# Kernel tuning notes

Hardware: AMD Instinct MI355X
Metric: run time of the kernel (lower is better)

The kernel has to match this reference:

```python
import jax, jax.numpy as jnp
import numpy as np

N, CIN, COUT, H, W = 32, 256, 256, 56, 56

def setup_inputs() -> dict:
    key = jax.random.key(0)
    k1, k2, k3 = jax.random.split(key, 3)
    x = jax.random.normal(k1, (N, CIN, H, W), dtype=jnp.float32)
    weight = jax.random.normal(k2, (COUT, CIN, 3, 3), dtype=jnp.float32) * 0.05
    bias = jax.random.normal(k3, (COUT,), dtype=jnp.float32)
    return {"x": x, "weight": weight, "bias": bias}

def reference(x, weight, bias):
    # 3x3 conv, stride=1, padding=1 (SAME), fused bias + ReLU.
    # Winograd F(2x2,3x3) is mathematically identical to direct conv.
    y = jax.lax.conv_general_dilated(
        x, weight,
        window_strides=(1, 1),
        padding=((1, 1), (1, 1)),
        dimension_numbers=("NCHW", "OIHW", "NCHW"),
    )
    return jax.nn.relu(y + bias[None, :, None, None])
```

## Files before the change

### kernel.cpp

```cpp
#include <hip/hip_runtime.h>


#define GLOBAL_AS __attribute__((address_space(1)))
#define LDS_AS __attribute__((address_space(3)))

typedef __attribute__((ext_vector_type(8))) short short8;
typedef __attribute__((ext_vector_type(4))) float f32x4;
typedef __attribute__((ext_vector_type(4))) unsigned int u32x4;

#define CIN   256
#define HWS   3136
#define PTOT  100352
#define KTOT  2304
#define WROWB 4608
#define ZPOFF 1179648
#define XTOFF 1310720
#define WSNEED (XTOFF + (size_t)PTOT * 512)

__device__ __forceinline__ unsigned short f2bf(float f) {
  unsigned u = __builtin_bit_cast(unsigned, f);
  return (unsigned short)((u + 0x7fffu + ((u >> 16) & 1u)) >> 16);
}

__global__ void wcvt_kernel(const float* __restrict__ w, unsigned char* __restrict__ ws) {
  if (blockIdx.x == 0 && threadIdx.x < 128)
    ((unsigned*)(ws + ZPOFF))[threadIdx.x] = 0u;
  int o = blockIdx.x * 256 + threadIdx.x;
  int co = o / KTOT;
  int rr = o - co * KTOT;
  int tap = rr >> 8;
  int ci = rr & 255;
  ((unsigned short*)ws)[o] = f2bf(w[co * KTOT + ci * 9 + tap]);
}

__global__ __launch_bounds__(256) void xcvt_kernel(const float* __restrict__ x,
                                                   unsigned char* __restrict__ ws) {
  __shared__ float lt[64 * 257];
  const int pg0 = blockIdx.x * 64;
  const int n   = pg0 / HWS;
  const int pi0 = pg0 - n * HWS;
  const int t   = threadIdx.x;
  {
    const int px = t & 63;
    const int cg = t >> 6;
    const float* xb = x + ((size_t)n * 256) * HWS + pi0 + px;
#pragma unroll 8
    for (int i = 0; i < 64; ++i) {
      const int c = i * 4 + cg;
      lt[px * 257 + c] = xb[(size_t)c * HWS];
    }
  }
  __syncthreads();
  {
    const int slot = t & 31;
    const int pxw  = t >> 5;
    unsigned char* xt = ws + XTOFF;
#pragma unroll
    for (int i = 0; i < 8; ++i) {
      const int p = i * 8 + pxw;
      const float* r = &lt[p * 257 + slot * 8];
      u32x4 v;
#pragma unroll
      for (int j = 0; j < 4; ++j)
        v[j] = (unsigned)f2bf(r[2 * j]) | ((unsigned)f2bf(r[2 * j + 1]) << 16);
      *(u32x4*)(xt + (size_t)(pg0 + p) * 512 + slot * 16) = v;
    }
  }
}

__global__ __launch_bounds__(256, 2) void conv_kernel(
    const unsigned char* __restrict__ ws, const float* __restrict__ bias,
    float* __restrict__ out) {
  __shared__ __align__(16) unsigned char smem[65536];

  const unsigned char* wb = ws;
  const unsigned char* xt = ws + XTOFF;
  const unsigned char* zp = ws + ZPOFF;

  const int bid = blockIdx.x;
  const int sw  = (bid & 7) * 196 + (bid >> 3);
  const int co0 = (sw & 1) * 128;
  const int p0  = (sw >> 1) * 128;

  const int t    = threadIdx.x;
  const int lane = t & 63;
  const int wave = t >> 6;
  const int wm   = wave & 1;
  const int wn   = wave >> 1;
  const int rl   = lane & 15;
  const int kq   = lane >> 4;
  const int l7   = lane & 7;
  const int l8   = lane >> 3;

  const unsigned chanoff = (unsigned)((l7 * 16) ^ ((l8 & 7) << 4));

  const unsigned char* aG[4];
  long long bG[4];
  int hB[4], wB[4];
#pragma unroll
  for (int i = 0; i < 4; ++i) {
    const int row = wave * 32 + i * 8 + l8;
    aG[i] = wb + (size_t)(co0 + row) * WROWB + chanoff;
    const int pg = p0 + row;
    const int n  = pg / HWS;
    const int pi = pg - n * HWS;
    hB[i] = pi / 56;
    wB[i] = pi - hB[i] * 56;
    bG[i] = (long long)pg * 512 + (long long)chanoff;
  }

  f32x4 acc[4][4];
  const f32x4 zero4 = {0.f, 0.f, 0.f, 0.f};
#pragma unroll
  for (int mi = 0; mi < 4; ++mi)
#pragma unroll
    for (int ni = 0; ni < 4; ++ni) acc[mi][ni] = zero4;

  auto stage = [&](int s, int buf) {
    const int cq  = s / 9;
    const int tap = s - cq * 9;
    const int kh  = tap / 3;
    const int dh  = kh - 1;
    const int dw  = (tap - kh * 3) - 1;
    const int koffA = tap * 512 + cq * 128;
    unsigned char* lb = smem + buf * 32768;
#pragma unroll
    for (int i = 0; i < 4; ++i) {
      __builtin_amdgcn_global_load_lds(
          (const GLOBAL_AS unsigned int*)(aG[i] + koffA),
          (LDS_AS unsigned int*)(lb + (wave * 4 + i) * 1024), 16, 0, 0);
    }
    const long long doff = (long long)(dh * 56 + dw) * 512 + cq * 128;
#pragma unroll
    for (int i = 0; i < 4; ++i) {
      const int hh = hB[i] + dh;
      const int wwi = wB[i] + dw;
      const bool ok = ((unsigned)hh < 56u) && ((unsigned)wwi < 56u);
      const unsigned char* g = ok ? (xt + bG[i] + doff) : zp;
      __builtin_amdgcn_global_load_lds(
          (const GLOBAL_AS unsigned int*)g,
          (LDS_AS unsigned int*)(lb + 16384 + (wave * 4 + i) * 1024), 16, 0, 0);
    }
  };

  unsigned offA[2], offB[2];
#pragma unroll
  for (int ks = 0; ks < 2; ++ks) {
    const unsigned koff = (unsigned)((kq * 16 + ks * 64) ^ (l7 << 4));
    offA[ks] = (unsigned)((wm * 64 + rl) * 128) + koff;
    offB[ks] = (unsigned)((wn * 64 + rl) * 128) + koff;
  }

  auto compute = [&](int buf) {
    const unsigned char* bA = smem + buf * 32768;
    const unsigned char* bB = bA + 16384;
#pragma unroll
    for (int ks = 0; ks < 2; ++ks) {
      short8 a[4], b[4];
#pragma unroll
      for (int mi = 0; mi < 4; ++mi)
        a[mi] = *(const short8*)(bA + offA[ks] + mi * 2048);
#pragma unroll
      for (int ni = 0; ni < 4; ++ni)
        b[ni] = *(const short8*)(bB + offB[ks] + ni * 2048);
#pragma unroll
      for (int mi = 0; mi < 4; ++mi)
#pragma unroll
        for (int ni = 0; ni < 4; ++ni)
          acc[mi][ni] = __builtin_amdgcn_mfma_f32_16x16x32_bf16(
              a[mi], b[ni], acc[mi][ni], 0, 0, 0);
    }
  };

  stage(0, 0);
  __syncthreads();
  int buf = 0;
  for (int s = 0; s < 36; ++s) {
    if (s < 35) stage(s + 1, buf ^ 1);
    compute(buf);
    __syncthreads();
    buf ^= 1;
  }

#pragma unroll
  for (int mi = 0; mi < 4; ++mi) {
    const int row = co0 + wm * 64 + mi * 16 + kq * 4;
    float br[4];
#pragma unroll
    for (int j = 0; j < 4; ++j) br[j] = bias[row + j];
#pragma unroll
    for (int ni = 0; ni < 4; ++ni) {
      const int pgb = p0 + wn * 64 + ni * 16;
      const int n   = pgb / HWS;
      const int pib = pgb - n * HWS;
#pragma unroll
      for (int j = 0; j < 4; ++j) {
        float v = acc[mi][ni][j] + br[j];
        out[(size_t)(n * 256 + row + j) * HWS + pib + rl] = fmaxf(v, 0.f);
      }
    }
  }
}

__global__ void naive_kernel(const float* __restrict__ x, const float* __restrict__ w,
                             const float* __restrict__ bias, float* __restrict__ out) {
  int idx = blockIdx.x * 256 + threadIdx.x;
  if (idx >= 32 * 256 * HWS) return;
  int n  = idx / (256 * HWS);
  int r  = idx - n * 256 * HWS;
  int co = r / HWS;
  int p  = r - co * HWS;
  int h = p / 56, ww = p - h * 56;
  float s = bias[co];
  const float* xb = x + (size_t)n * 256 * HWS;
  const float* wbp = w + (size_t)co * KTOT;
  for (int ci = 0; ci < 256; ++ci) {
    const float* xc = xb + (size_t)ci * HWS;
    const float* wc = wbp + ci * 9;
    for (int kh = 0; kh < 3; ++kh) {
      int hh = h + kh - 1;
      if ((unsigned)hh >= 56u) continue;
      for (int kw = 0; kw < 3; ++kw) {
        int w2 = ww + kw - 1;
        if ((unsigned)w2 >= 56u) continue;
        s += xc[hh * 56 + w2] * wc[kh * 3 + kw];
      }
    }
  }
  out[idx] = fmaxf(s, 0.f);
}

extern "C" void kernel_launch(void* const* d_in, const int* in_sizes, int n_in,
                              void* d_out, int out_size, void* d_ws, size_t ws_size,
                              hipStream_t stream) {
  const float* x    = (const float*)d_in[0];
  const float* w    = (const float*)d_in[1];
  const float* bias = (const float*)d_in[2];
  float* out        = (float*)d_out;

  if (ws_size < WSNEED) {
    hipLaunchKernelGGL(naive_kernel, dim3((32 * 256 * HWS + 255) / 256), dim3(256),
                       0, stream, x, w, bias, out);
    return;
  }
  unsigned char* ws = (unsigned char*)d_ws;
  hipLaunchKernelGGL(wcvt_kernel, dim3(2304), dim3(256), 0, stream, w, ws);
  hipLaunchKernelGGL(xcvt_kernel, dim3(PTOT / 64), dim3(256), 0, stream, x, ws);
  hipLaunchKernelGGL(conv_kernel, dim3(1568), dim3(256), 0, stream, ws, bias, out);
}
```

Baseline: 169.0 us.

## Deepen conv pipeline to 4 stages with half-size K chunks and setprio

Splits each K stage from 128 to 64 bytes per row (72 stages instead of 36) and replaces the double-buffered loop with a 4-buffer ring that prefetches three stages ahead. Each step uses explicit vmcnt waits plus s_barrier in place of __syncthreads, and wraps the MFMA block in s_setprio. The LDS swizzle and load mapping are rewritten for the 64-byte rows. The aim is to hide global-to-LDS latency more deeply and cut barrier stalls, at the cost of twice as many barriers and smaller MFMA bursts per sync.

```diff
diff --git a/kernel.cpp b/kernel.cpp
--- a/kernel.cpp
+++ b/kernel.cpp
@@ -89,24 +89,23 @@
   const int wn   = wave >> 1;
   const int rl   = lane & 15;
   const int kq   = lane >> 4;
-  const int l7   = lane & 7;
-  const int l8   = lane >> 3;
-
-  const unsigned chanoff = (unsigned)((l7 * 16) ^ ((l8 & 7) << 4));
-
-  const unsigned char* aG[4];
-  long long bG[4];
-  int hB[4], wB[4];
-#pragma unroll
-  for (int i = 0; i < 4; ++i) {
-    const int row = wave * 32 + i * 8 + l8;
-    aG[i] = wb + (size_t)(co0 + row) * WROWB + chanoff;
+  const int q2   = lane >> 2;
+
+  const unsigned jb = (unsigned)(((lane & 3) ^ ((lane >> 3) & 3)) * 16);
+
+  const unsigned char* aG[2];
+  long long bG[2];
+  int hB[2], wB[2];
+#pragma unroll
+  for (int i = 0; i < 2; ++i) {
+    const int row = i * 64 + wave * 16 + q2;
+    aG[i] = wb + (size_t)(co0 + row) * WROWB + jb;
     const int pg = p0 + row;
     const int n  = pg / HWS;
     const int pi = pg - n * HWS;
     hB[i] = pi / 56;
     wB[i] = pi - hB[i] * 56;
-    bG[i] = (long long)pg * 512 + (long long)chanoff;
+    bG[i] = (long long)pg * 512 + (long long)jb;
   }
 
   f32x4 acc[4][4];
@@ -122,65 +121,67 @@
     const int kh  = tap / 3;
     const int dh  = kh - 1;
     const int dw  = (tap - kh * 3) - 1;
-    const int koffA = tap * 512 + cq * 128;
-    unsigned char* lb = smem + buf * 32768;
-#pragma unroll
-    for (int i = 0; i < 4; ++i) {
+    const unsigned koffA = (unsigned)(tap * 512 + cq * 64);
+    unsigned char* lbA = smem + buf * 8192 + wave * 1024;
+    unsigned char* lbB = smem + 32768 + buf * 8192 + wave * 1024;
+#pragma unroll
+    for (int i = 0; i < 2; ++i)
       __builtin_amdgcn_global_load_lds(
           (const GLOBAL_AS unsigned int*)(aG[i] + koffA),
-          (LDS_AS unsigned int*)(lb + (wave * 4 + i) * 1024), 16, 0, 0);
-    }
-    const long long doff = (long long)(dh * 56 + dw) * 512 + cq * 128;
-#pragma unroll
-    for (int i = 0; i < 4; ++i) {
-      const int hh = hB[i] + dh;
+          (LDS_AS unsigned int*)(lbA + i * 4096), 16, 0, 0);
+    const long long doff = (long long)(dh * 56 + dw) * 512 + cq * 64;
+#pragma unroll
+    for (int i = 0; i < 2; ++i) {
+      const int hh  = hB[i] + dh;
       const int wwi = wB[i] + dw;
       const bool ok = ((unsigned)hh < 56u) && ((unsigned)wwi < 56u);
       const unsigned char* g = ok ? (xt + bG[i] + doff) : zp;
       __builtin_amdgcn_global_load_lds(
           (const GLOBAL_AS unsigned int*)g,
-          (LDS_AS unsigned int*)(lb + 16384 + (wave * 4 + i) * 1024), 16, 0, 0);
+          (LDS_AS unsigned int*)(lbB + i * 4096), 16, 0, 0);
     }
   };
 
-  unsigned offA[2], offB[2];
-#pragma unroll
-  for (int ks = 0; ks < 2; ++ks) {
-    const unsigned koff = (unsigned)((kq * 16 + ks * 64) ^ (l7 << 4));
-    offA[ks] = (unsigned)((wm * 64 + rl) * 128) + koff;
-    offB[ks] = (unsigned)((wn * 64 + rl) * 128) + koff;
-  }
-
-  auto compute = [&](int buf) {
-    const unsigned char* bA = smem + buf * 32768;
-    const unsigned char* bB = bA + 16384;
-#pragma unroll
-    for (int ks = 0; ks < 2; ++ks) {
-      short8 a[4], b[4];
-#pragma unroll
-      for (int mi = 0; mi < 4; ++mi)
-        a[mi] = *(const short8*)(bA + offA[ks] + mi * 2048);
-#pragma unroll
-      for (int ni = 0; ni < 4; ++ni)
-        b[ni] = *(const short8*)(bB + offB[ks] + ni * 2048);
-#pragma unroll
-      for (int mi = 0; mi < 4; ++mi)
-#pragma unroll
-        for (int ni = 0; ni < 4; ++ni)
-          acc[mi][ni] = __builtin_amdgcn_mfma_f32_16x16x32_bf16(
-              a[mi], b[ni], acc[mi][ni], 0, 0, 0);
-    }
-  };
+  const unsigned srd  = (unsigned)((kq ^ ((rl >> 1) & 3)) * 16);
+  const unsigned offA = (unsigned)((wm * 64 + rl) * 64) + srd;
+  const unsigned offB = (unsigned)((wn * 64 + rl) * 64) + srd;
+
+#define STEP(S, BUF, VM, DO_STAGE)                                           \
+  {                                                                          \
+    asm volatile("s_waitcnt vmcnt(" VM ")\n\ts_barrier" ::: "memory");       \
+    const unsigned char* bA = smem + (BUF) * 8192;                           \
+    const unsigned char* bB = smem + 32768 + (BUF) * 8192;                   \
+    short8 av[4], bv[4];                                                     \
+    _Pragma("unroll") for (int mi = 0; mi < 4; ++mi)                         \
+        av[mi] = *(const short8*)(bA + offA + mi * 1024);                    \
+    _Pragma("unroll") for (int ni = 0; ni < 4; ++ni)                         \
+        bv[ni] = *(const short8*)(bB + offB + ni * 1024);                    \
+    if (DO_STAGE) stage((S) + 3, ((S) + 3) & 3);                             \
+    __builtin_amdgcn_s_setprio(1);                                           \
+    _Pragma("unroll") for (int mi = 0; mi < 4; ++mi)                         \
+      _Pragma("unroll") for (int ni = 0; ni < 4; ++ni)                       \
+          acc[mi][ni] = __builtin_amdgcn_mfma_f32_16x16x32_bf16(             \
+              av[mi], bv[ni], acc[mi][ni], 0, 0, 0);                         \
+    __builtin_amdgcn_s_setprio(0);                                           \
+  }
 
   stage(0, 0);
-  __syncthreads();
-  int buf = 0;
-  for (int s = 0; s < 36; ++s) {
-    if (s < 35) stage(s + 1, buf ^ 1);
-    compute(buf);
-    __syncthreads();
-    buf ^= 1;
-  }
+  stage(1, 1);
+  stage(2, 2);
+
+#pragma unroll 1
+  for (int qq = 0; qq < 17; ++qq) {
+    const int s = qq * 4;
+    STEP(s + 0, 0, "8", true)
+    STEP(s + 1, 1, "8", true)
+    STEP(s + 2, 2, "8", true)
+    STEP(s + 3, 3, "8", true)
+  }
+  STEP(68, 0, "8", true)
+  STEP(69, 1, "8", false)
+  STEP(70, 2, "4", false)
+  STEP(71, 3, "0", false)
+#undef STEP
 
 #pragma unroll
   for (int mi = 0; mi < 4; ++mi) {
```

New measurement: 182.6 us. 8.1% more time.

## Pre-swizzle weights into MFMA fragment layout and load A directly to registers

Applied to the files above, without the earlier changes.

The weight conversion kernel now writes bf16 weights already arranged in the per-lane MFMA A-fragment order. The conv kernel loads A operands straight from global memory into registers, double-buffered across pipeline stages, instead of staging them through LDS. LDS use is halved, leaving only the activation tile, which cuts LDS traffic and may allow higher occupancy. The cost is more register pressure from two A register sets and A loads with global latency inside the main loop.

```diff
diff --git a/kernel.cpp b/kernel.cpp
--- a/kernel.cpp
+++ b/kernel.cpp
@@ -12,7 +12,6 @@
 #define HWS   3136
 #define PTOT  100352
 #define KTOT  2304
-#define WROWB 4608
 #define ZPOFF 1179648
 #define XTOFF 1310720
 #define WSNEED (XTOFF + (size_t)PTOT * 512)
@@ -25,12 +24,28 @@
 __global__ void wcvt_kernel(const float* __restrict__ w, unsigned char* __restrict__ ws) {
   if (blockIdx.x == 0 && threadIdx.x < 128)
     ((unsigned*)(ws + ZPOFF))[threadIdx.x] = 0u;
-  int o = blockIdx.x * 256 + threadIdx.x;
-  int co = o / KTOT;
-  int rr = o - co * KTOT;
-  int tap = rr >> 8;
-  int ci = rr & 255;
-  ((unsigned short*)ws)[o] = f2bf(w[co * KTOT + ci * 9 + tap]);
+  const int tid = blockIdx.x * 256 + threadIdx.x;
+  const int l   = tid & 63;
+  const int fi  = tid >> 6;
+  const int ks  = fi & 1;
+  const int t2  = fi >> 1;
+  const int g   = t2 / 36;
+  const int s   = t2 - g * 36;
+  const int cq  = s / 9;
+  const int tap = s - cq * 9;
+  const int rl  = l & 15;
+  const int kq  = l >> 4;
+  const int co  = g * 16 + rl;
+  const int ci0 = cq * 64 + ks * 32 + kq * 8;
+  const float* src = w + (size_t)co * KTOT + tap;
+  u32x4 v;
+#pragma unroll
+  for (int j = 0; j < 4; ++j) {
+    unsigned lo = f2bf(src[(size_t)(ci0 + 2 * j) * 9]);
+    unsigned hi = f2bf(src[(size_t)(ci0 + 2 * j + 1) * 9]);
+    v[j] = lo | (hi << 16);
+  }
+  *(u32x4*)(ws + (size_t)tid * 16) = v;
 }
 
 __global__ __launch_bounds__(256) void xcvt_kernel(const float* __restrict__ x,
@@ -71,9 +86,9 @@
 __global__ __launch_bounds__(256, 2) void conv_kernel(
     const unsigned char* __restrict__ ws, const float* __restrict__ bias,
     float* __restrict__ out) {
-  __shared__ __align__(16) unsigned char smem[65536];
-
-  const unsigned char* wb = ws;
+  __shared__ __align__(16) unsigned char smem[32768];
+
+  const unsigned char* wf = ws;
   const unsigned char* xt = ws + XTOFF;
   const unsigned char* zp = ws + ZPOFF;
 
@@ -92,15 +107,19 @@
   const int l7   = lane & 7;
   const int l8   = lane >> 3;
 
+  const unsigned char* aW[4];
+#pragma unroll
+  for (int mi = 0; mi < 4; ++mi) {
+    const int g = (co0 >> 4) + wm * 4 + mi;
+    aW[mi] = wf + (size_t)g * 73728 + (size_t)lane * 16;
+  }
+
   const unsigned chanoff = (unsigned)((l7 * 16) ^ ((l8 & 7) << 4));
-
-  const unsigned char* aG[4];
   long long bG[4];
   int hB[4], wB[4];
 #pragma unroll
   for (int i = 0; i < 4; ++i) {
     const int row = wave * 32 + i * 8 + l8;
-    aG[i] = wb + (size_t)(co0 + row) * WROWB + chanoff;
     const int pg = p0 + row;
     const int n  = pg / HWS;
     const int pi = pg - n * HWS;
@@ -122,64 +141,69 @@
     const int kh  = tap / 3;
     const int dh  = kh - 1;
     const int dw  = (tap - kh * 3) - 1;
-    const int koffA = tap * 512 + cq * 128;
-    unsigned char* lb = smem + buf * 32768;
+    unsigned char* lb = smem + buf * 16384;
+    const long long doff = (long long)(dh * 56 + dw) * 512 + cq * 128;
 #pragma unroll
     for (int i = 0; i < 4; ++i) {
-      __builtin_amdgcn_global_load_lds(
-          (const GLOBAL_AS unsigned int*)(aG[i] + koffA),
-          (LDS_AS unsigned int*)(lb + (wave * 4 + i) * 1024), 16, 0, 0);
-    }
-    const long long doff = (long long)(dh * 56 + dw) * 512 + cq * 128;
-#pragma unroll
-    for (int i = 0; i < 4; ++i) {
-      const int hh = hB[i] + dh;
+      const int hh  = hB[i] + dh;
       const int wwi = wB[i] + dw;
       const bool ok = ((unsigned)hh < 56u) && ((unsigned)wwi < 56u);
       const unsigned char* g = ok ? (xt + bG[i] + doff) : zp;
       __builtin_amdgcn_global_load_lds(
           (const GLOBAL_AS unsigned int*)g,
-          (LDS_AS unsigned int*)(lb + 16384 + (wave * 4 + i) * 1024), 16, 0, 0);
+          (LDS_AS unsigned int*)(lb + (wave * 4 + i) * 1024), 16, 0, 0);
     }
   };
 
-  unsigned offA[2], offB[2];
-#pragma unroll
-  for (int ks = 0; ks < 2; ++ks) {
-    const unsigned koff = (unsigned)((kq * 16 + ks * 64) ^ (l7 << 4));
-    offA[ks] = (unsigned)((wm * 64 + rl) * 128) + koff;
-    offB[ks] = (unsigned)((wn * 64 + rl) * 128) + koff;
-  }
-
-  auto compute = [&](int buf) {
-    const unsigned char* bA = smem + buf * 32768;
-    const unsigned char* bB = bA + 16384;
+  auto aload = [&](int s, short8* dst) {
+#pragma unroll
+    for (int ks = 0; ks < 2; ++ks)
+#pragma unroll
+      for (int mi = 0; mi < 4; ++mi)
+        dst[ks * 4 + mi] =
+            *(const short8*)(aW[mi] + (unsigned)((s * 2 + ks) * 1024));
+  };
+
+  unsigned offB[2];
+#pragma unroll
+  for (int ks = 0; ks < 2; ++ks)
+    offB[ks] = (unsigned)((wn * 64 + rl) * 128) +
+               (unsigned)((kq * 16 + ks * 64) ^ (l7 << 4));
+
+  auto compute = [&](int buf, const short8* av) {
+    const unsigned char* bB = smem + buf * 16384;
 #pragma unroll
     for (int ks = 0; ks < 2; ++ks) {
-      short8 a[4], b[4];
-#pragma unroll
-      for (int mi = 0; mi < 4; ++mi)
-        a[mi] = *(const short8*)(bA + offA[ks] + mi * 2048);
+      short8 bv[4];
 #pragma unroll
       for (int ni = 0; ni < 4; ++ni)
-        b[ni] = *(const short8*)(bB + offB[ks] + ni * 2048);
+        bv[ni] = *(const short8*)(bB + offB[ks] + ni * 2048);
 #pragma unroll
       for (int mi = 0; mi < 4; ++mi)
 #pragma unroll
         for (int ni = 0; ni < 4; ++ni)
           acc[mi][ni] = __builtin_amdgcn_mfma_f32_16x16x32_bf16(
-              a[mi], b[ni], acc[mi][ni], 0, 0, 0);
+              av[ks * 4 + mi], bv[ni], acc[mi][ni], 0, 0, 0);
     }
   };
 
+  short8 aregA[8], aregB[8];
+  aload(0, aregA);
   stage(0, 0);
   __syncthreads();
-  int buf = 0;
-  for (int s = 0; s < 36; ++s) {
-    if (s < 35) stage(s + 1, buf ^ 1);
-    compute(buf);
+#pragma unroll 1
+  for (int qq = 0; qq < 18; ++qq) {
+    const int s = qq * 2;
+    stage(s + 1, 1);
+    aload(s + 1, aregB);
+    compute(0, aregA);
     __syncthreads();
-    buf ^= 1;
+    if (s + 2 < 36) {
+      stage(s + 2, 0);
+      aload(s + 2, aregA);
+    }
+    compute(1, aregB);
+    __syncthreads();
   }
 
 #pragma unroll
@@ -244,7 +268,7 @@
     return;
   }
   unsigned char* ws = (unsigned char*)d_ws;
-  hipLaunchKernelGGL(wcvt_kernel, dim3(2304), dim3(256), 0, stream, w, ws);
+  hipLaunchKernelGGL(wcvt_kernel, dim3(288), dim3(256), 0, stream, w, ws);
   hipLaunchKernelGGL(xcvt_kernel, dim3(PTOT / 64), dim3(256), 0, stream, x, ws);
   hipLaunchKernelGGL(conv_kernel, dim3(1568), dim3(256), 0, stream, ws, bias, out);
 }
```

Result: slower. 256.5 us (+51.8%).

## Enlarge conv tile to 256x256 with 512-thread blocks and prioritized MFMA scheduling

Applied to the files above, without the earlier changes.

The implicit-GEMM conv block now covers all 256 output channels and 256 pixels using 8 waves and 128 KB of double-buffered LDS, so each block loads the input and weight tiles once instead of twice. The main loop is split into cq and tap loops with explicit vmcnt waits and barriers. Fragment loads are interleaved with MFMA groups under s_setprio to overlap LDS reads with matrix work. The costs are a grid of only 392 blocks, so most likely one block per CU, higher accumulator register pressure, and wave imbalance across CUs.

```diff
diff --git a/kernel.cpp b/kernel.cpp
--- a/kernel.cpp
+++ b/kernel.cpp
@@ -68,19 +68,18 @@
   }
 }
 
-__global__ __launch_bounds__(256, 2) void conv_kernel(
+__global__ __launch_bounds__(512, 2) void conv_kernel(
     const unsigned char* __restrict__ ws, const float* __restrict__ bias,
     float* __restrict__ out) {
-  __shared__ __align__(16) unsigned char smem[65536];
+  __shared__ __align__(16) unsigned char smem[131072];
 
   const unsigned char* wb = ws;
   const unsigned char* xt = ws + XTOFF;
   const unsigned char* zp = ws + ZPOFF;
 
   const int bid = blockIdx.x;
-  const int sw  = (bid & 7) * 196 + (bid >> 3);
-  const int co0 = (sw & 1) * 128;
-  const int p0  = (sw >> 1) * 128;
+  const int sw  = (bid & 7) * 49 + (bid >> 3);
+  const int p0  = sw * 256;
 
   const int t    = threadIdx.x;
   const int lane = t & 63;
@@ -90,101 +89,143 @@
   const int rl   = lane & 15;
   const int kq   = lane >> 4;
   const int l7   = lane & 7;
-  const int l8   = lane >> 3;
-
-  const unsigned chanoff = (unsigned)((l7 * 16) ^ ((l8 & 7) << 4));
+
+  const int srow = t >> 3;
+  const unsigned swzs = (unsigned)(((t & 7) * 16) ^ ((srow & 7) << 4));
+  const unsigned ldsW = (unsigned)(wave * 1024);
 
   const unsigned char* aG[4];
   long long bG[4];
-  int hB[4], wB[4];
-#pragma unroll
-  for (int i = 0; i < 4; ++i) {
-    const int row = wave * 32 + i * 8 + l8;
-    aG[i] = wb + (size_t)(co0 + row) * WROWB + chanoff;
-    const int pg = p0 + row;
+  int hB[4], wBp[4];
+#pragma unroll
+  for (int op = 0; op < 4; ++op) {
+    const int arow = op * 64 + srow;
+    aG[op] = wb + (size_t)arow * WROWB + swzs;
+    const int pg = p0 + op * 64 + srow;
     const int n  = pg / HWS;
     const int pi = pg - n * HWS;
-    hB[i] = pi / 56;
-    wB[i] = pi - hB[i] * 56;
-    bG[i] = (long long)pg * 512 + (long long)chanoff;
-  }
-
-  f32x4 acc[4][4];
+    hB[op]  = pi / 56;
+    wBp[op] = pi - hB[op] * 56;
+    bG[op]  = (long long)pg * 512 + (long long)swzs;
+  }
+
+  f32x4 acc[8][4];
   const f32x4 zero4 = {0.f, 0.f, 0.f, 0.f};
 #pragma unroll
-  for (int mi = 0; mi < 4; ++mi)
+  for (int mi = 0; mi < 8; ++mi)
 #pragma unroll
     for (int ni = 0; ni < 4; ++ni) acc[mi][ni] = zero4;
 
-  auto stage = [&](int s, int buf) {
-    const int cq  = s / 9;
-    const int tap = s - cq * 9;
-    const int kh  = tap / 3;
-    const int dh  = kh - 1;
-    const int dw  = (tap - kh * 3) - 1;
-    const int koffA = tap * 512 + cq * 128;
-    unsigned char* lb = smem + buf * 32768;
-#pragma unroll
-    for (int i = 0; i < 4; ++i) {
+  auto stage = [&](int cq, int tap, int buf) {
+    const int kh = tap / 3;
+    const int dh = kh - 1;
+    const int dw = (tap - kh * 3) - 1;
+    const unsigned koffA = (unsigned)(tap * 512 + cq * 128);
+    unsigned char* lb = smem + buf * 65536;
+#pragma unroll
+    for (int op = 0; op < 4; ++op)
       __builtin_amdgcn_global_load_lds(
-          (const GLOBAL_AS unsigned int*)(aG[i] + koffA),
-          (LDS_AS unsigned int*)(lb + (wave * 4 + i) * 1024), 16, 0, 0);
-    }
+          (const GLOBAL_AS unsigned int*)(aG[op] + koffA),
+          (LDS_AS unsigned int*)(lb + op * 8192 + ldsW), 16, 0, 0);
     const long long doff = (long long)(dh * 56 + dw) * 512 + cq * 128;
 #pragma unroll
-    for (int i = 0; i < 4; ++i) {
-      const int hh = hB[i] + dh;
-      const int wwi = wB[i] + dw;
+    for (int op = 0; op < 4; ++op) {
+      const int hh  = hB[op] + dh;
+      const int wwi = wBp[op] + dw;
       const bool ok = ((unsigned)hh < 56u) && ((unsigned)wwi < 56u);
-      const unsigned char* g = ok ? (xt + bG[i] + doff) : zp;
+      const unsigned char* g = ok ? (xt + bG[op] + doff) : zp;
       __builtin_amdgcn_global_load_lds(
           (const GLOBAL_AS unsigned int*)g,
-          (LDS_AS unsigned int*)(lb + 16384 + (wave * 4 + i) * 1024), 16, 0, 0);
+          (LDS_AS unsigned int*)(lb + 32768 + op * 8192 + ldsW), 16, 0, 0);
     }
   };
 
-  unsigned offA[2], offB[2];
-#pragma unroll
-  for (int ks = 0; ks < 2; ++ks) {
-    const unsigned koff = (unsigned)((kq * 16 + ks * 64) ^ (l7 << 4));
-    offA[ks] = (unsigned)((wm * 64 + rl) * 128) + koff;
-    offB[ks] = (unsigned)((wn * 64 + rl) * 128) + koff;
-  }
-
-  auto compute = [&](int buf) {
-    const unsigned char* bA = smem + buf * 32768;
-    const unsigned char* bB = bA + 16384;
-#pragma unroll
-    for (int ks = 0; ks < 2; ++ks) {
-      short8 a[4], b[4];
-#pragma unroll
-      for (int mi = 0; mi < 4; ++mi)
-        a[mi] = *(const short8*)(bA + offA[ks] + mi * 2048);
+  unsigned koff[2];
+  koff[0] = (unsigned)((kq * 16) ^ (l7 << 4));
+  koff[1] = (unsigned)((kq * 16 + 64) ^ (l7 << 4));
+  unsigned offAm[8], offBn[4];
+#pragma unroll
+  for (int mi = 0; mi < 8; ++mi)
+    offAm[mi] = (unsigned)((wm * 128 + mi * 16 + rl) * 128);
+#pragma unroll
+  for (int ni = 0; ni < 4; ++ni)
+    offBn[ni] = (unsigned)((wn * 64 + ni * 16 + rl) * 128);
+
+  stage(0, 0, 0);
+
+  int buf = 0;
+#pragma unroll 1
+  for (int cq = 0; cq < 4; ++cq) {
+#pragma unroll 1
+    for (int tap = 0; tap < 9; ++tap) {
+      asm volatile("s_waitcnt vmcnt(0)\n\ts_barrier" ::: "memory");
+      if (!((cq == 3) && (tap == 8))) {
+        const int ntap = (tap == 8) ? 0 : tap + 1;
+        const int ncq  = (tap == 8) ? cq + 1 : cq;
+        stage(ncq, ntap, buf ^ 1);
+      }
+      const unsigned char* bA = smem + buf * 65536;
+      const unsigned char* bB = bA + 32768;
+
+      short8 bv[4], av[4];
 #pragma unroll
       for (int ni = 0; ni < 4; ++ni)
-        b[ni] = *(const short8*)(bB + offB[ks] + ni * 2048);
+        bv[ni] = *(const short8*)(bB + offBn[ni] + koff[0]);
+#pragma unroll
+      for (int mi = 0; mi < 4; ++mi)
+        av[mi] = *(const short8*)(bA + offAm[mi] + koff[0]);
+      __builtin_amdgcn_s_setprio(1);
 #pragma unroll
       for (int mi = 0; mi < 4; ++mi)
 #pragma unroll
         for (int ni = 0; ni < 4; ++ni)
           acc[mi][ni] = __builtin_amdgcn_mfma_f32_16x16x32_bf16(
-              a[mi], b[ni], acc[mi][ni], 0, 0, 0);
-    }
-  };
-
-  stage(0, 0);
-  __syncthreads();
-  int buf = 0;
-  for (int s = 0; s < 36; ++s) {
-    if (s < 35) stage(s + 1, buf ^ 1);
-    compute(buf);
-    __syncthreads();
-    buf ^= 1;
-  }
-
-#pragma unroll
-  for (int mi = 0; mi < 4; ++mi) {
-    const int row = co0 + wm * 64 + mi * 16 + kq * 4;
+              av[mi], bv[ni], acc[mi][ni], 0, 0, 0);
+      __builtin_amdgcn_s_setprio(0);
+#pragma unroll
+      for (int mi = 0; mi < 4; ++mi)
+        av[mi] = *(const short8*)(bA + offAm[mi + 4] + koff[0]);
+      __builtin_amdgcn_s_setprio(1);
+#pragma unroll
+      for (int mi = 0; mi < 4; ++mi)
+#pragma unroll
+        for (int ni = 0; ni < 4; ++ni)
+          acc[mi + 4][ni] = __builtin_amdgcn_mfma_f32_16x16x32_bf16(
+              av[mi], bv[ni], acc[mi + 4][ni], 0, 0, 0);
+      __builtin_amdgcn_s_setprio(0);
+#pragma unroll
+      for (int ni = 0; ni < 4; ++ni)
+        bv[ni] = *(const short8*)(bB + offBn[ni] + koff[1]);
+#pragma unroll
+      for (int mi = 0; mi < 4; ++mi)
+        av[mi] = *(const short8*)(bA + offAm[mi] + koff[1]);
+      __builtin_amdgcn_s_setprio(1);
+#pragma unroll
+      for (int mi = 0; mi < 4; ++mi)
+#pragma unroll
+        for (int ni = 0; ni < 4; ++ni)
+          acc[mi][ni] = __builtin_amdgcn_mfma_f32_16x16x32_bf16(
+              av[mi], bv[ni], acc[mi][ni], 0, 0, 0);
+      __builtin_amdgcn_s_setprio(0);
+#pragma unroll
+      for (int mi = 0; mi < 4; ++mi)
+        av[mi] = *(const short8*)(bA + offAm[mi + 4] + koff[1]);
+      __builtin_amdgcn_s_setprio(1);
+#pragma unroll
+      for (int mi = 0; mi < 4; ++mi)
+#pragma unroll
+        for (int ni = 0; ni < 4; ++ni)
+          acc[mi + 4][ni] = __builtin_amdgcn_mfma_f32_16x16x32_bf16(
+              av[mi], bv[ni], acc[mi + 4][ni], 0, 0, 0);
+      __builtin_amdgcn_s_setprio(0);
+
+      buf ^= 1;
+    }
+  }
+
+#pragma unroll
+  for (int mi = 0; mi < 8; ++mi) {
+    const int row = wm * 128 + mi * 16 + kq * 4;
     float br[4];
 #pragma unroll
     for (int j = 0; j < 4; ++j) br[j] = bias[row + j];
@@ -246,5 +287,5 @@
   unsigned char* ws = (unsigned char*)d_ws;
   hipLaunchKernelGGL(wcvt_kernel, dim3(2304), dim3(256), 0, stream, w, ws);
   hipLaunchKernelGGL(xcvt_kernel, dim3(PTOT / 64), dim3(256), 0, stream, x, ws);
-  hipLaunchKernelGGL(conv_kernel, dim3(1568), dim3(256), 0, stream, ws, bias, out);
-}
+  hipLaunchKernelGGL(conv_kernel, dim3(392), dim3(512), 0, stream, ws, bias, out);
+}
```

New measurement: 163.5 us. 1.03x faster.
